# Optimization experiments

Hardware: AMD Instinct MI355X
Metric: run time of the kernel (lower is better)

The kernel has to match this reference:

```python
import jax, jax.numpy as jnp
import numpy as np

NEG_BIG = -9e15
ALPHA = 0.2  # leaky relu slope

def setup_inputs() -> dict:
    key = jax.random.key(0)
    k1, k2, k3, k4, k5 = jax.random.split(key, 5)
    N, F_in, F_out, H = 4096, 512, 64, 8
    x = jax.random.normal(k1, (N, F_in), dtype=jnp.float32)
    adj = jax.random.randint(k2, (N, N), 0, 2, dtype=jnp.int32)
    W = jax.random.normal(k3, (H, F_in, F_out), dtype=jnp.float32) * (1.414 * (2.0 / (F_in + F_out)) ** 0.5)
    a_source = jax.random.normal(k4, (H, 1, F_out), dtype=jnp.float32) * (1.414 * (2.0 / (1 + F_out)) ** 0.5)
    a_target = jax.random.normal(k5, (H, 1, F_out), dtype=jnp.float32) * (1.414 * (2.0 / (1 + F_out)) ** 0.5)
    return {"x": x, "adj": adj, "W": W, "a_source": a_source, "a_target": a_target}

def reference(x, adj, W, a_source, a_target):
    # Wh: [H, N, F_out]
    Wh = jnp.einsum('nf,hfo->hno', x, W)
    # additive attention logits
    s_i = jnp.sum(a_source * Wh, axis=2, keepdims=True)          # [H, N, 1]
    s_j = jnp.sum(a_target * Wh, axis=2, keepdims=True)          # [H, N, 1]
    e = s_i + jnp.swapaxes(s_j, 1, 2)                            # [H, N, N]
    e = jnp.where(e > 0, e, ALPHA * e)                           # leaky relu
    e = jnp.where(adj[None] > 0, e, jnp.float32(NEG_BIG))        # adjacency mask
    attention = jax.nn.softmax(e, axis=2)                        # [H, N, N]
    h_prime = jnp.einsum('hij,hjo->hio', attention, Wh)          # [H, N, F_out]
    return h_prime
```

## Files before the change

### kernel.cpp

```cpp
#include <hip/hip_runtime.h>
#include <hip/hip_fp16.h>
#include <cstdint>

#define N_NODES 4096
#define F_IN    512
#define F_OUT   64
#define H_HEADS 8
#define JC      4

constexpr float L2E = 1.44269504088896f;

typedef _Float16 half2_t __attribute__((ext_vector_type(2)));
typedef _Float16 half4_t __attribute__((ext_vector_type(4)));
typedef _Float16 half8_t __attribute__((ext_vector_type(8)));
typedef float    f32x4   __attribute__((ext_vector_type(4)));

__device__ inline unsigned int exp2_pk_u(unsigned int au) {
    __half2 h = __builtin_bit_cast(__half2, au);
    h = h2exp2(h);
    return __builtin_bit_cast(unsigned int, h);
}

__global__ __launch_bounds__(256) void k_prep(const int* __restrict__ adj,
                                              const float* __restrict__ W,
                                              unsigned long long* __restrict__ adjwT,
                                              _Float16* __restrict__ wfrag) {
    if (blockIdx.x < 128) {
        int gid = blockIdx.x * 256 + threadIdx.x;
        int h     = gid >> 12;
        int kt    = (gid >> 8) & 15;
        int ntile = (gid >> 6) & 3;
        int lane  = gid & 63;
        int c0 = lane & 15, g = lane >> 4;
        const float* src = W + ((size_t)h * F_IN + kt * 32 + 8 * g) * F_OUT + ntile * 16 + c0;
        half8_t hv;
        #pragma unroll
        for (int t = 0; t < 8; t++) hv[t] = (_Float16)src[(size_t)t * F_OUT];
        *reinterpret_cast<half8_t*>(&wfrag[(size_t)gid * 8]) = hv;
        return;
    }
    int bid  = blockIdx.x - 128;
    int lane = threadIdx.x & 63;
    int wid  = (int)((bid * 256 + threadIdx.x) >> 6);
    int nwaves = (2048 * 256) >> 6;
    const int nchunks = N_NODES * (N_NODES / 64);
    for (int cf = wid; cf < nchunks; cf += nwaves) {
        int v = adj[(size_t)cf * 64 + lane];
        unsigned long long mask = __ballot(v > 0);
        if (lane == 0) {
            int i = cf >> 6, c = cf & 63;
            adjwT[(size_t)c * N_NODES + i] = mask;
        }
    }
}

__global__ __launch_bounds__(512) void k_wh_mfma(const float* __restrict__ x,
                                                 const _Float16* __restrict__ wfrag,
                                                 const float* __restrict__ a_src,
                                                 const float* __restrict__ a_tgt,
                                                 _Float16* __restrict__ WhFrag,
                                                 float* __restrict__ s_iL,
                                                 _Float16* __restrict__ s_jLh) {
    __shared__ f32x4 red[4][4][64];
    const int h    = blockIdx.y;
    const int rt   = blockIdx.x;
    const int t    = threadIdx.x;
    const int lane = t & 63;
    const int w    = t >> 6;
    const int mtw  = w & 3;
    const int kh   = w >> 2;
    const int mt   = rt * 4 + mtw;
    const int c0   = lane & 15;
    const int gl   = lane >> 4;

    f32x4 acc0 = {0.f, 0.f, 0.f, 0.f};
    f32x4 acc1 = {0.f, 0.f, 0.f, 0.f};
    f32x4 acc2 = {0.f, 0.f, 0.f, 0.f};
    f32x4 acc3 = {0.f, 0.f, 0.f, 0.f};

    const float* __restrict__ xr = x + (size_t)(mt * 16 + c0) * F_IN + 8 * gl + kh * 256;
    const _Float16* __restrict__ Bf = wfrag + (size_t)h * (16 * 4 * 512)
                                    + (size_t)kh * 8 * 2048 + (size_t)lane * 8;

    #pragma unroll
    for (int kt = 0; kt < 8; kt++) {
        float4 v0 = *reinterpret_cast<const float4*>(xr + kt * 32);
        float4 v1 = *reinterpret_cast<const float4*>(xr + kt * 32 + 4);
        half8_t a;
        a[0] = (_Float16)v0.x; a[1] = (_Float16)v0.y; a[2] = (_Float16)v0.z; a[3] = (_Float16)v0.w;
        a[4] = (_Float16)v1.x; a[5] = (_Float16)v1.y; a[6] = (_Float16)v1.z; a[7] = (_Float16)v1.w;
        const _Float16* Bk = Bf + (size_t)kt * 2048;
        half8_t b0 = *reinterpret_cast<const half8_t*>(Bk);
        half8_t b1 = *reinterpret_cast<const half8_t*>(Bk + 512);
        half8_t b2 = *reinterpret_cast<const half8_t*>(Bk + 1024);
        half8_t b3 = *reinterpret_cast<const half8_t*>(Bk + 1536);
        acc0 = __builtin_amdgcn_mfma_f32_16x16x32_f16(a, b0, acc0, 0, 0, 0);
        acc1 = __builtin_amdgcn_mfma_f32_16x16x32_f16(a, b1, acc1, 0, 0, 0);
        acc2 = __builtin_amdgcn_mfma_f32_16x16x32_f16(a, b2, acc2, 0, 0, 0);
        acc3 = __builtin_amdgcn_mfma_f32_16x16x32_f16(a, b3, acc3, 0, 0, 0);
    }

    if (kh == 1) {
        red[mtw][0][lane] = acc0;
        red[mtw][1][lane] = acc1;
        red[mtw][2][lane] = acc2;
        red[mtw][3][lane] = acc3;
    }
    __syncthreads();
    if (kh == 1) return;

    acc0 += red[mtw][0][lane];
    acc1 += red[mtw][1][lane];
    acc2 += red[mtw][2][lane];
    acc3 += red[mtw][3][lane];

    const float as0 = a_src[h * 64 + c0],      at0 = a_tgt[h * 64 + c0];
    const float as1 = a_src[h * 64 + 16 + c0], at1 = a_tgt[h * 64 + 16 + c0];
    const float as2 = a_src[h * 64 + 32 + c0], at2 = a_tgt[h * 64 + 32 + c0];
    const float as3 = a_src[h * 64 + 48 + c0], at3 = a_tgt[h * 64 + 48 + c0];

    #pragma unroll
    for (int reg = 0; reg < 4; reg++) {
        float vi = acc0[reg] * as0 + acc1[reg] * as1 + acc2[reg] * as2 + acc3[reg] * as3;
        float vj = acc0[reg] * at0 + acc1[reg] * at1 + acc2[reg] * at2 + acc3[reg] * at3;
        #pragma unroll
        for (int mm = 8; mm >= 1; mm >>= 1) {
            vi += __shfl_xor(vi, mm, 64);
            vj += __shfl_xor(vj, mm, 64);
        }
        if (c0 == 0) {
            int row = mt * 16 + 4 * gl + reg;
            s_iL[h * N_NODES + row]  = vi * L2E;
            s_jLh[h * N_NODES + row] = (_Float16)(vj * L2E);
        }
    }

    const int cc    = mt >> 2;
    const int kb    = (mt >> 1) & 1;
    const int lanep = c0 + 16 * ((mt & 1) * 2 + (gl >> 1));
    const int tb    = 4 * (gl & 1);
    _Float16* dst = WhFrag + (size_t)h * (N_NODES * 64)
                  + (size_t)(cc * 2 + kb) * 2048 + (size_t)lanep * 8 + tb;
    f32x4 accs[4] = {acc0, acc1, acc2, acc3};
    #pragma unroll
    for (int ot = 0; ot < 4; ot++) {
        half4_t hv;
        #pragma unroll
        for (int reg = 0; reg < 4; reg++) hv[reg] = (_Float16)accs[ot][reg];
        *reinterpret_cast<half4_t*>(dst + ot * 512) = hv;
    }
}

__global__ __launch_bounds__(256) void k_hmax(const _Float16* __restrict__ s_jLh,
                                              float* __restrict__ mxAll) {
    __shared__ float red[4];
    const int h = blockIdx.x;
    const int t = threadIdx.x;
    const _Float16* p = s_jLh + h * N_NODES;
    float m = -INFINITY;
    for (int k = t; k < N_NODES; k += 256) m = fmaxf(m, (float)p[k]);
    #pragma unroll
    for (int mm = 32; mm >= 1; mm >>= 1) m = fmaxf(m, __shfl_xor(m, mm, 64));
    if ((t & 63) == 0) red[t >> 6] = m;
    __syncthreads();
    if (t == 0) mxAll[h] = fmaxf(fmaxf(red[0], red[1]), fmaxf(red[2], red[3]));
}

__global__ __launch_bounds__(256, 4) void k_attn_mfma(const _Float16* __restrict__ WhFrag,
                                                      const float* __restrict__ s_iL,
                                                      const float* __restrict__ mxAll,
                                                      const _Float16* __restrict__ s_jLh,
                                                      const unsigned long long* __restrict__ adjwT,
                                                      float* __restrict__ out0,
                                                      _Float16* __restrict__ partH,
                                                      float* __restrict__ lbuf) {
    __shared__ uint2 ktab4[16];
    __shared__ _Float16 Bs[2][4096];
    if (threadIdx.x < 16) {
        unsigned int nib = threadIdx.x;
        unsigned int w0 = ((nib & 1u) ? 0xFFFFu : 0u) | ((nib & 2u) ? 0xFFFF0000u : 0u);
        unsigned int w1 = ((nib & 4u) ? 0xFFFFu : 0u) | ((nib & 8u) ? 0xFFFF0000u : 0u);
        ktab4[nib] = make_uint2(w0, w1);
    }

    const int tid  = threadIdx.x;
    const int h    = blockIdx.y;
    const int jc   = blockIdx.z;
    const int lane = tid & 63;
    const int w    = tid >> 6;
    const int i0   = blockIdx.x * 128 + w * 32;
    const int mrow = lane & 15;
    const int gl   = lane >> 4;
    const int gl8  = gl << 3;

    const float siL0 = s_iL[h * N_NODES + i0 + mrow];
    const float siL1 = s_iL[h * N_NODES + i0 + 16 + mrow];
    const float mxh  = mxAll[h];
    const float tm0 = siL0 + mxh, tm1 = siL1 + mxh;
    const float m0 = fmaxf(tm0, 0.2f * tm0);
    const float m1 = fmaxf(tm1, 0.2f * tm1);
    const half2_t u2_0 = {(_Float16)(siL0 - m0), (_Float16)(siL0 - m0)};
    const half2_t u2_1 = {(_Float16)(siL1 - m1), (_Float16)(siL1 - m1)};
    const half2_t n82_0 = {(_Float16)(-0.8f * m0), (_Float16)(-0.8f * m0)};
    const half2_t n82_1 = {(_Float16)(-0.8f * m1), (_Float16)(-0.8f * m1)};
    const half2_t c02 = {(_Float16)0.2f, (_Float16)0.2f};

    const _Float16* __restrict__ sjh = s_jLh + h * N_NODES;
    const _Float16* __restrict__ Bh  = WhFrag + (size_t)h * (N_NODES * 64);

    half8_t vone;
    #pragma unroll
    for (int q = 0; q < 8; q++) vone[q] = (_Float16)1.0f;

    f32x4 accA0 = {0,0,0,0}, accA1 = {0,0,0,0}, accA2 = {0,0,0,0}, accA3 = {0,0,0,0};
    f32x4 accB0 = {0,0,0,0}, accB1 = {0,0,0,0}, accB2 = {0,0,0,0}, accB3 = {0,0,0,0};
    f32x4 acclA = {0,0,0,0}, acclB = {0,0,0,0};

    const int NC   = (N_NODES / 64) / JC;
    const int cbeg = jc * NC;
    const int cend = cbeg + NC;

    {
        const _Float16* src = Bh + (size_t)cbeg * 4096 + tid * 8;
        *reinterpret_cast<half8_t*>(&Bs[0][tid * 8])        = *reinterpret_cast<const half8_t*>(src);
        *reinterpret_cast<half8_t*>(&Bs[0][2048 + tid * 8]) = *reinterpret_cast<const half8_t*>(src + 2048);
    }
    __syncthreads();

    int cur = 0;
    for (int c = cbeg; c < cend; c++) {
        half8_t n0, n1;
        const bool hasNext = (c + 1 < cend);
        if (hasNext) {
            const _Float16* src = Bh + (size_t)(c + 1) * 4096 + tid * 8;
            n0 = *reinterpret_cast<const half8_t*>(src);
            n1 = *reinterpret_cast<const half8_t*>(src + 2048);
        }

        uint2 word0 = *reinterpret_cast<const uint2*>(&adjwT[(size_t)c * N_NODES + i0 + mrow]);
        uint2 word1 = *reinterpret_cast<const uint2*>(&adjwT[(size_t)c * N_NODES + i0 + 16 + mrow]);

        #pragma unroll
        for (int kb = 0; kb < 2; kb++) {
            const int jb = c * 64 + kb * 32 + 8 * gl;
            half8_t sjv = *reinterpret_cast<const half8_t*>(&sjh[jb]);
            unsigned int bm0 = ((kb ? word0.y : word0.x) >> gl8) & 0xFFu;
            unsigned int bm1 = ((kb ? word1.y : word1.x) >> gl8) & 0xFFu;
            uint2 klo0 = ktab4[bm0 & 15u], khi0 = ktab4[bm0 >> 4];
            uint2 klo1 = ktab4[bm1 & 15u], khi1 = ktab4[bm1 >> 4];
            uint4 mk0 = {klo0.x, klo0.y, khi0.x, khi0.y};
            uint4 mk1 = {klo1.x, klo1.y, khi1.x, khi1.y};

            uint4 sju = __builtin_bit_cast(uint4, sjv);
            uint4 p0u, p1u;
            #pragma unroll
            for (int q = 0; q < 4; q++) {
                unsigned int sw = (q == 0) ? sju.x : (q == 1) ? sju.y : (q == 2) ? sju.z : sju.w;
                half2_t sj2 = __builtin_bit_cast(half2_t, sw);
                half2_t a1 = u2_0 + sj2;
                half2_t am = __builtin_elementwise_max(a1, a1 * c02 + n82_0);
                unsigned int pa = exp2_pk_u(__builtin_bit_cast(unsigned int, am));
                half2_t b1 = u2_1 + sj2;
                half2_t bmv = __builtin_elementwise_max(b1, b1 * c02 + n82_1);
                unsigned int pb = exp2_pk_u(__builtin_bit_cast(unsigned int, bmv));
                unsigned int ka  = (q == 0) ? mk0.x : (q == 1) ? mk0.y : (q == 2) ? mk0.z : mk0.w;
                unsigned int kbm = (q == 0) ? mk1.x : (q == 1) ? mk1.y : (q == 2) ? mk1.z : mk1.w;
                pa &= ka; pb &= kbm;
                if (q == 0) { p0u.x = pa; p1u.x = pb; }
                else if (q == 1) { p0u.y = pa; p1u.y = pb; }
                else if (q == 2) { p0u.z = pa; p1u.z = pb; }
                else { p0u.w = pa; p1u.w = pb; }
            }
            half8_t af0 = __builtin_bit_cast(half8_t, p0u);
            half8_t af1 = __builtin_bit_cast(half8_t, p1u);

            const _Float16* Bk = &Bs[cur][kb * 2048 + lane * 8];
            half8_t b0  = *reinterpret_cast<const half8_t*>(Bk);
            half8_t b1v = *reinterpret_cast<const half8_t*>(Bk + 512);
            half8_t b2  = *reinterpret_cast<const half8_t*>(Bk + 1024);
            half8_t b3  = *reinterpret_cast<const half8_t*>(Bk + 1536);

            accA0 = __builtin_amdgcn_mfma_f32_16x16x32_f16(af0, b0,  accA0, 0, 0, 0);
            accB0 = __builtin_amdgcn_mfma_f32_16x16x32_f16(af1, b0,  accB0, 0, 0, 0);
            accA1 = __builtin_amdgcn_mfma_f32_16x16x32_f16(af0, b1v, accA1, 0, 0, 0);
            accB1 = __builtin_amdgcn_mfma_f32_16x16x32_f16(af1, b1v, accB1, 0, 0, 0);
            accA2 = __builtin_amdgcn_mfma_f32_16x16x32_f16(af0, b2,  accA2, 0, 0, 0);
            accB2 = __builtin_amdgcn_mfma_f32_16x16x32_f16(af1, b2,  accB2, 0, 0, 0);
            accA3 = __builtin_amdgcn_mfma_f32_16x16x32_f16(af0, b3,  accA3, 0, 0, 0);
            accB3 = __builtin_amdgcn_mfma_f32_16x16x32_f16(af1, b3,  accB3, 0, 0, 0);
            acclA = __builtin_amdgcn_mfma_f32_16x16x32_f16(af0, vone, acclA, 0, 0, 0);
            acclB = __builtin_amdgcn_mfma_f32_16x16x32_f16(af1, vone, acclB, 0, 0, 0);
        }

        if (hasNext) {
            *reinterpret_cast<half8_t*>(&Bs[cur ^ 1][tid * 8])        = n0;
            *reinterpret_cast<half8_t*>(&Bs[cur ^ 1][2048 + tid * 8]) = n1;
        }
        __syncthreads();
        cur ^= 1;
    }

    float* lp = lbuf + (size_t)jc * (H_HEADS * N_NODES);
    if (mrow == 0) {
        #pragma unroll
        for (int r = 0; r < 4; r++) {
            lp[h * N_NODES + i0 + 4 * gl + r]      = acclA[r];
            lp[h * N_NODES + i0 + 16 + 4 * gl + r] = acclB[r];
        }
    }
    if (jc == 0) {
        #pragma unroll
        for (int r = 0; r < 4; r++) {
            size_t obA = ((size_t)h * N_NODES + i0 + 4 * gl + r) * 64 + mrow;
            size_t obB = ((size_t)h * N_NODES + i0 + 16 + 4 * gl + r) * 64 + mrow;
            out0[obA + 0]  = accA0[r];
            out0[obA + 16] = accA1[r];
            out0[obA + 32] = accA2[r];
            out0[obA + 48] = accA3[r];
            out0[obB + 0]  = accB0[r];
            out0[obB + 16] = accB1[r];
            out0[obB + 32] = accB2[r];
            out0[obB + 48] = accB3[r];
        }
    } else {
        _Float16* op = partH + (size_t)(jc - 1) * ((size_t)H_HEADS * N_NODES * F_OUT);
        #pragma unroll
        for (int r = 0; r < 4; r++) {
            size_t obA = ((size_t)h * N_NODES + i0 + 4 * gl + r) * 64 + mrow;
            size_t obB = ((size_t)h * N_NODES + i0 + 16 + 4 * gl + r) * 64 + mrow;
            op[obA + 0]  = (_Float16)accA0[r];
            op[obA + 16] = (_Float16)accA1[r];
            op[obA + 32] = (_Float16)accA2[r];
            op[obA + 48] = (_Float16)accA3[r];
            op[obB + 0]  = (_Float16)accB0[r];
            op[obB + 16] = (_Float16)accB1[r];
            op[obB + 32] = (_Float16)accB2[r];
            op[obB + 48] = (_Float16)accB3[r];
        }
    }
}

__global__ __launch_bounds__(256) void k_norm(float* __restrict__ out,
                                              const _Float16* __restrict__ partH,
                                              const float* __restrict__ lbuf) {
    const int HN = H_HEADS * N_NODES;
    int idx = blockIdx.x * 256 + threadIdx.x;
    int row = idx >> 4;
    float inv = 1.0f / (lbuf[row] + lbuf[HN + row] + lbuf[2 * HN + row] + lbuf[3 * HN + row]);
    float4 a = reinterpret_cast<const float4*>(out)[idx];
    float s0 = a.x, s1 = a.y, s2 = a.z, s3 = a.w;
    #pragma unroll
    for (int p = 0; p < 3; p++) {
        half4_t hp = *reinterpret_cast<const half4_t*>(
            &partH[(size_t)p * ((size_t)H_HEADS * N_NODES * F_OUT) + (size_t)idx * 4]);
        s0 += (float)hp[0]; s1 += (float)hp[1]; s2 += (float)hp[2]; s3 += (float)hp[3];
    }
    float4 v = {s0 * inv, s1 * inv, s2 * inv, s3 * inv};
    reinterpret_cast<float4*>(out)[idx] = v;
}

extern "C" void kernel_launch(void* const* d_in, const int* in_sizes, int n_in,
                              void* d_out, int out_size, void* d_ws, size_t ws_size,
                              hipStream_t stream) {
    const float* x     = (const float*)d_in[0];
    const int*   adj   = (const int*)d_in[1];
    const float* W     = (const float*)d_in[2];
    const float* a_src = (const float*)d_in[3];
    const float* a_tgt = (const float*)d_in[4];
    float* out = (float*)d_out;

    char* ws = (char*)d_ws;
    size_t off = 0;
    auto alloc = [&](size_t bytes) -> char* {
        char* p = ws + off;
        off += (bytes + 255) & ~(size_t)255;
        return p;
    };
    _Float16* WhFrag = (_Float16*)alloc((size_t)H_HEADS * N_NODES * F_OUT * 2);
    _Float16* wfrag  = (_Float16*)alloc((size_t)H_HEADS * 16 * 4 * 64 * 8 * 2);
    float* s_iL      = (float*)alloc((size_t)H_HEADS * N_NODES * 4);
    _Float16* s_jLh  = (_Float16*)alloc((size_t)H_HEADS * N_NODES * 2);
    float* mxAll     = (float*)alloc((size_t)H_HEADS * 4);
    float* lbuf      = (float*)alloc((size_t)JC * H_HEADS * N_NODES * 4);
    _Float16* partH  = (_Float16*)alloc((size_t)(JC - 1) * H_HEADS * N_NODES * F_OUT * 2);
    unsigned long long* adjwT = (unsigned long long*)alloc((size_t)N_NODES * (N_NODES / 64) * 8);
    (void)ws_size;

    k_prep<<<2176, 256, 0, stream>>>(adj, W, adjwT, wfrag);
    k_wh_mfma<<<dim3(N_NODES / 64, H_HEADS), 512, 0, stream>>>(x, wfrag, a_src, a_tgt,
                                                               WhFrag, s_iL, s_jLh);
    k_hmax<<<H_HEADS, 256, 0, stream>>>(s_jLh, mxAll);
    k_attn_mfma<<<dim3(N_NODES / 128, H_HEADS, JC), 256, 0, stream>>>(WhFrag, s_iL, mxAll, s_jLh,
                                                                      adjwT, out, partH, lbuf);
    k_norm<<<(H_HEADS * N_NODES * F_OUT / 4) / 256, 256, 0, stream>>>(out, partH, lbuf);
}
```

Before: 80.75 us.

## Stage x tile in LDS once and share across all heads in Wh GEMM

The Wh projection kernel now assigns one block per 16-row tile, and each of its 8 waves handles one head. The x rows are converted to fp16 once and stored in a swizzled LDS buffer. Previously each head's block reloaded and reconverted x from global memory and split K across two waves with an LDS reduction. The new layout removes the redundant x traffic and the reduction step, but each wave now runs a longer serial K loop and the grid is 256 blocks instead of 512.

```diff
diff --git a/kernel.cpp b/kernel.cpp
--- a/kernel.cpp
+++ b/kernel.cpp
@@ -61,34 +61,45 @@
                                                  _Float16* __restrict__ WhFrag,
                                                  float* __restrict__ s_iL,
                                                  _Float16* __restrict__ s_jLh) {
-    __shared__ f32x4 red[4][4][64];
-    const int h    = blockIdx.y;
+    __shared__ _Float16 xs[16 * 512];
     const int rt   = blockIdx.x;
     const int t    = threadIdx.x;
     const int lane = t & 63;
-    const int w    = t >> 6;
-    const int mtw  = w & 3;
-    const int kh   = w >> 2;
-    const int mt   = rt * 4 + mtw;
+    const int h    = t >> 6;
     const int c0   = lane & 15;
     const int gl   = lane >> 4;
+
+    {
+        const int srow = t >> 5;
+        const int seg  = t & 31;
+        const float* src = x + (size_t)(rt * 16 + srow) * F_IN + seg * 16;
+        _Float16* drow = &xs[srow * 512];
+        #pragma unroll
+        for (int j = 0; j < 2; j++) {
+            float4 v0 = *reinterpret_cast<const float4*>(src + j * 8);
+            float4 v1 = *reinterpret_cast<const float4*>(src + j * 8 + 4);
+            half8_t hv;
+            hv[0] = (_Float16)v0.x; hv[1] = (_Float16)v0.y; hv[2] = (_Float16)v0.z; hv[3] = (_Float16)v0.w;
+            hv[4] = (_Float16)v1.x; hv[5] = (_Float16)v1.y; hv[6] = (_Float16)v1.z; hv[7] = (_Float16)v1.w;
+            int u  = seg * 2 + j;
+            int up = u ^ (srow & 7);
+            *reinterpret_cast<half8_t*>(&drow[up * 8]) = hv;
+        }
+    }
+    __syncthreads();
 
     f32x4 acc0 = {0.f, 0.f, 0.f, 0.f};
     f32x4 acc1 = {0.f, 0.f, 0.f, 0.f};
     f32x4 acc2 = {0.f, 0.f, 0.f, 0.f};
     f32x4 acc3 = {0.f, 0.f, 0.f, 0.f};
 
-    const float* __restrict__ xr = x + (size_t)(mt * 16 + c0) * F_IN + 8 * gl + kh * 256;
-    const _Float16* __restrict__ Bf = wfrag + (size_t)h * (16 * 4 * 512)
-                                    + (size_t)kh * 8 * 2048 + (size_t)lane * 8;
-
-    #pragma unroll
-    for (int kt = 0; kt < 8; kt++) {
-        float4 v0 = *reinterpret_cast<const float4*>(xr + kt * 32);
-        float4 v1 = *reinterpret_cast<const float4*>(xr + kt * 32 + 4);
-        half8_t a;
-        a[0] = (_Float16)v0.x; a[1] = (_Float16)v0.y; a[2] = (_Float16)v0.z; a[3] = (_Float16)v0.w;
-        a[4] = (_Float16)v1.x; a[5] = (_Float16)v1.y; a[6] = (_Float16)v1.z; a[7] = (_Float16)v1.w;
+    const _Float16* __restrict__ Bf   = wfrag + (size_t)h * (16 * 4 * 512) + (size_t)lane * 8;
+    const _Float16* __restrict__ arow = &xs[c0 * 512];
+
+    #pragma unroll
+    for (int kt = 0; kt < 16; kt++) {
+        int up = (kt * 4 + gl) ^ (c0 & 7);
+        half8_t a = *reinterpret_cast<const half8_t*>(&arow[up * 8]);
         const _Float16* Bk = Bf + (size_t)kt * 2048;
         half8_t b0 = *reinterpret_cast<const half8_t*>(Bk);
         half8_t b1 = *reinterpret_cast<const half8_t*>(Bk + 512);
@@ -100,20 +111,6 @@
         acc3 = __builtin_amdgcn_mfma_f32_16x16x32_f16(a, b3, acc3, 0, 0, 0);
     }
 
-    if (kh == 1) {
-        red[mtw][0][lane] = acc0;
-        red[mtw][1][lane] = acc1;
-        red[mtw][2][lane] = acc2;
-        red[mtw][3][lane] = acc3;
-    }
-    __syncthreads();
-    if (kh == 1) return;
-
-    acc0 += red[mtw][0][lane];
-    acc1 += red[mtw][1][lane];
-    acc2 += red[mtw][2][lane];
-    acc3 += red[mtw][3][lane];
-
     const float as0 = a_src[h * 64 + c0],      at0 = a_tgt[h * 64 + c0];
     const float as1 = a_src[h * 64 + 16 + c0], at1 = a_tgt[h * 64 + 16 + c0];
     const float as2 = a_src[h * 64 + 32 + c0], at2 = a_tgt[h * 64 + 32 + c0];
@@ -129,15 +126,15 @@
             vj += __shfl_xor(vj, mm, 64);
         }
         if (c0 == 0) {
-            int row = mt * 16 + 4 * gl + reg;
+            int row = rt * 16 + 4 * gl + reg;
             s_iL[h * N_NODES + row]  = vi * L2E;
             s_jLh[h * N_NODES + row] = (_Float16)(vj * L2E);
         }
     }
 
-    const int cc    = mt >> 2;
-    const int kb    = (mt >> 1) & 1;
-    const int lanep = c0 + 16 * ((mt & 1) * 2 + (gl >> 1));
+    const int cc    = rt >> 2;
+    const int kb    = (rt >> 1) & 1;
+    const int lanep = c0 + 16 * ((rt & 1) * 2 + (gl >> 1));
     const int tb    = 4 * (gl & 1);
     _Float16* dst = WhFrag + (size_t)h * (N_NODES * 64)
                   + (size_t)(cc * 2 + kb) * 2048 + (size_t)lanep * 8 + tb;
@@ -387,8 +384,7 @@
     (void)ws_size;
 
     k_prep<<<2176, 256, 0, stream>>>(adj, W, adjwT, wfrag);
-    k_wh_mfma<<<dim3(N_NODES / 64, H_HEADS), 512, 0, stream>>>(x, wfrag, a_src, a_tgt,
-                                                               WhFrag, s_iL, s_jLh);
+    k_wh_mfma<<<N_NODES / 16, 512, 0, stream>>>(x, wfrag, a_src, a_tgt, WhFrag, s_iL, s_jLh);
     k_hmax<<<H_HEADS, 256, 0, stream>>>(s_jLh, mxAll);
     k_attn_mfma<<<dim3(N_NODES / 128, H_HEADS, JC), 256, 0, stream>>>(WhFrag, s_iL, mxAll, s_jLh,
                                                                       adjwT, out, partH, lbuf);
```

Result: faster. 77.06 us (-4.6%).
